# Optimization experiments

Hardware: AMD Instinct MI355X
Metric: run time of the kernel (lower is better)

The kernel has to match this reference:

```python
import jax, jax.numpy as jnp
import numpy as np

N = 100_000      # nodes
E = 1_600_000    # directed edges (before self-loops)
G = 128          # graphs in batch
IN = 32          # in_channels
HID = 32         # hidden_channels (per head)
HEADS = 4
SLOPE = 0.2      # GATConv leaky_relu negative_slope


def setup_inputs() -> dict:
    key = jax.random.key(0)
    ks = jax.random.split(key, 12)
    x = jax.random.normal(ks[0], (N, IN), jnp.float32)
    edge_index = jax.random.randint(ks[1], (2, E), 0, N)
    batch = jnp.sort(jax.random.randint(ks[2], (N,), 0, G))
    g = lambda k, sh: jax.random.normal(k, sh, jnp.float32) * (1.0 / np.sqrt(sh[0]))
    return {
        "x": x, "edge_index": edge_index, "batch": batch,
        # conv1: in -> heads*hid, concat
        "W1": g(ks[3], (IN, HEADS * HID)),
        "a_src1": jax.random.normal(ks[4], (HEADS, HID), jnp.float32) * 0.1,
        "a_dst1": jax.random.normal(ks[5], (HEADS, HID), jnp.float32) * 0.1,
        "b1": jnp.zeros((HEADS * HID,), jnp.float32),
        # conv2: heads*hid -> hid, heads=1, mean (concat=False)
        "W2": g(ks[6], (HEADS * HID, 1 * HID)),
        "a_src2": jax.random.normal(ks[7], (1, HID), jnp.float32) * 0.1,
        "a_dst2": jax.random.normal(ks[8], (1, HID), jnp.float32) * 0.1,
        "b2": jnp.zeros((HID,), jnp.float32),
        # classifier
        "Wc": g(ks[9], (HID, 1)),
        "bc": jnp.zeros((1,), jnp.float32),
    }


def _segment_softmax(e, seg, n):
    # e: [E', H]; softmax over edges sharing the same destination node
    m = jax.ops.segment_max(e, seg, num_segments=n)
    ex = jnp.exp(e - m[seg])
    den = jax.ops.segment_sum(ex, seg, num_segments=n)
    return ex / den[seg]


def _gat_layer(x, src, dst, W, a_src, a_dst, b, heads, ch, concat):
    n = x.shape[0]
    h = (x @ W).reshape(n, heads, ch)              # [N, H, C]
    e_src = jnp.sum(h * a_src, axis=-1)            # [N, H]
    e_dst = jnp.sum(h * a_dst, axis=-1)            # [N, H]
    e = jax.nn.leaky_relu(e_src[src] + e_dst[dst], SLOPE)   # [E', H]
    alpha = _segment_softmax(e, dst, n)            # [E', H]
    msg = h[src] * alpha[:, :, None]               # [E', H, C]
    out = jax.ops.segment_sum(msg, dst, num_segments=n)     # [N, H, C]
    out = out.reshape(n, heads * ch) if concat else out.mean(axis=1)
    return out + b


def reference(x, edge_index, batch, W1, a_src1, a_dst1, b1, W2, a_src2, a_dst2, b2, Wc, bc):
    n = x.shape[0]
    loops = jnp.arange(n, dtype=edge_index.dtype)  # GATConv add_self_loops=True
    src = jnp.concatenate([edge_index[0], loops])
    dst = jnp.concatenate([edge_index[1], loops])
    h = jax.nn.elu(_gat_layer(x, src, dst, W1, a_src1, a_dst1, b1, HEADS, HID, True))
    # dropout: eval mode -> identity
    h = jax.nn.elu(_gat_layer(h, src, dst, W2, a_src2, a_dst2, b2, 1, HID, False))
    # global_mean_pool over batch ids
    sums = jax.ops.segment_sum(h, batch, num_segments=G)
    cnt = jax.ops.segment_sum(jnp.ones((n, 1), h.dtype), batch, num_segments=G)
    pooled = sums / jnp.maximum(cnt, 1.0)
    return pooled @ Wc + bc                        # [G, 1]
```

## Files before the change

kernel.cpp:

```cpp
#include <hip/hip_runtime.h>
#include <math.h>

#define NT 100000
#define ET 1600000
#define GT 128
#define NBK 391
#define BSH 8
#define NBLK_A 256
#define CHUNK_A 6250

typedef float f4 __attribute__((ext_vector_type(4)));

__device__ __forceinline__ float lrelu(float v) { return v > 0.0f ? v : 0.2f * v; }
__device__ __forceinline__ float elu1(float v) { return v > 0.0f ? v : __expf(v) - 1.0f; }

__global__ __launch_bounds__(256) void k_histA(const int* __restrict__ dst, int* __restrict__ histA) {
  __shared__ int histL[NBK];
  int t = threadIdx.x, blk = blockIdx.x;
  for (int i = t; i < NBK; i += 256) histL[i] = 0;
  __syncthreads();
  int e0 = blk * CHUNK_A, e1 = min(ET, e0 + CHUNK_A);
  for (int e = e0 + t; e < e1; e += 256) atomicAdd(&histL[dst[e] >> BSH], 1);
  __syncthreads();
  for (int i = t; i < NBK; i += 256) histA[i * NBLK_A + blk] = histL[i];
}

__global__ __launch_bounds__(256) void k_scanB(int* __restrict__ histA, int* __restrict__ btot) {
  __shared__ int sh[256];
  int b = blockIdx.x, t = threadIdx.x;
  int v = histA[b * NBLK_A + t];
  sh[t] = v;
  __syncthreads();
  for (int off = 1; off < 256; off <<= 1) {
    int xv = (t >= off) ? sh[t - off] : 0;
    __syncthreads();
    sh[t] += xv;
    __syncthreads();
  }
  histA[b * NBLK_A + t] = sh[t] - v;
  if (t == 255) btot[b] = sh[255];
}

__global__ __launch_bounds__(512) void k_scanC(const int* __restrict__ btot, int* __restrict__ bbase) {
  __shared__ int sh[512];
  int t = threadIdx.x;
  int v = (t < NBK) ? btot[t] : 0;
  sh[t] = v;
  __syncthreads();
  for (int off = 1; off < 512; off <<= 1) {
    int xv = (t >= off) ? sh[t - off] : 0;
    __syncthreads();
    sh[t] += xv;
    __syncthreads();
  }
  if (t < NBK) bbase[t] = sh[t] - v;
  if (t == 0) bbase[NBK] = ET;
}

__global__ __launch_bounds__(256) void k_buck(const int* __restrict__ src, const int* __restrict__ dst,
                                              const int* __restrict__ histA, const int* __restrict__ bbase,
                                              int2* __restrict__ ebuf) {
  __shared__ int cur[NBK];
  int t = threadIdx.x, blk = blockIdx.x;
  for (int i = t; i < NBK; i += 256) cur[i] = histA[i * NBLK_A + blk] + bbase[i];
  __syncthreads();
  int e0 = blk * CHUNK_A, e1 = min(ET, e0 + CHUNK_A);
  for (int e = e0 + t; e < e1; e += 256) {
    int s = src[e], d = dst[e];
    int pos = atomicAdd(&cur[d >> BSH], 1);
    ebuf[pos] = make_int2(s, d);
  }
}

__global__ __launch_bounds__(256) void k_fine(const int2* __restrict__ ebuf, const int* __restrict__ bbase,
                                              int* __restrict__ rp, int* __restrict__ adj) {
  __shared__ int cnt[256];
  __shared__ int sh[256];
  __shared__ int cur[256];
  int b = blockIdx.x, t = threadIdx.x;
  int eb0 = bbase[b], eb1 = bbase[b + 1];
  cnt[t] = 0;
  __syncthreads();
  for (int e = eb0 + t; e < eb1; e += 256) atomicAdd(&cnt[ebuf[e].y & 255], 1);
  __syncthreads();
  int v = cnt[t];
  sh[t] = v;
  __syncthreads();
  for (int off = 1; off < 256; off <<= 1) {
    int xv = (t >= off) ? sh[t - off] : 0;
    __syncthreads();
    sh[t] += xv;
    __syncthreads();
  }
  int start = eb0 + sh[t] - v;
  cur[t] = start;
  int node = (b << BSH) + t;
  if (node < NT) rp[node] = start;
  if (node == NT - 1) rp[NT] = ET;
  __syncthreads();
  for (int e = eb0 + t; e < eb1; e += 256) {
    int2 p = ebuf[e];
    int pos = atomicAdd(&cur[p.y & 255], 1);
    adj[pos] = p.x;
  }
}

__global__ void k_prep(const float* __restrict__ W1, const float* __restrict__ as1,
                       const float* __restrict__ ad1, float* __restrict__ AB) {
  int t = threadIdx.x;
  int k = t >> 3, j = t & 7;
  const float* a = (j < 4) ? as1 : ad1;
  int h = j & 3;
  float s = 0.0f;
  for (int c = 0; c < 32; ++c) s += W1[k * 128 + h * 32 + c] * a[h * 32 + c];
  AB[t] = s;
}

__global__ __launch_bounds__(256) void k_att1(const float* __restrict__ x, const float* __restrict__ AB,
                                              float* __restrict__ es, float* __restrict__ ed) {
  __shared__ float xsh[32 * 33];
  __shared__ float absh[256];
  int t = threadIdx.x;
  int n0 = blockIdx.x * 32;
  absh[t] = AB[t];
  for (int i = t; i < 1024; i += 256) {
    int ln = i >> 5, k = i & 31;
    int node = n0 + ln;
    xsh[ln * 33 + k] = (node < NT) ? x[node * 32 + k] : 0.0f;
  }
  __syncthreads();
  int ln = t >> 3, j = t & 7;
  int node = n0 + ln;
  if (node < NT) {
    float s = 0.0f;
#pragma unroll
    for (int k = 0; k < 32; ++k) s += xsh[ln * 33 + k] * absh[k * 8 + j];
    if (j < 4) es[node * 4 + j] = s;
    else ed[node * 4 + (j - 4)] = s;
  }
}

__global__ __launch_bounds__(256) void k_agg1f(
    const int* __restrict__ rp, const int* __restrict__ adj,
    const float* __restrict__ es, const float* __restrict__ ed,
    const float* __restrict__ x,
    const float* __restrict__ W1, const float* __restrict__ b1,
    const float* __restrict__ W2,
    const float* __restrict__ as2, const float* __restrict__ ad2,
    float* __restrict__ h2, float* __restrict__ es2, float* __restrict__ ed2) {
  __shared__ int sbuf[8][34];
  __shared__ f4 wbufv[8][34];
  __shared__ float ysh[8][132];
  __shared__ float osh[8][132];
  int t = threadIdx.x;
  int wv = t >> 6, l = t & 63;
  int g = l >> 5, j = l & 31;
  int ns = wv * 2 + g;
  int n = blockIdx.x * 8 + ns;
  bool valid = (n < NT);
  int nc = valid ? n : NT - 1;
  const f4* es4 = (const f4*)es;
  int rs = rp[nc], re = rp[nc + 1];
  int deg = re - rs;
  f4 edn = ((const f4*)ed)[nc];
  f4 esn = es4[nc];
  float sv[4];
#pragma unroll
  for (int h = 0; h < 4; ++h) sv[h] = __expf(lrelu(esn[h] + edn[h]));
  int eg2 = j >> 3, q = j & 7;
  f4 a0 = {0,0,0,0}, a1 = {0,0,0,0}, a2 = {0,0,0,0}, a3 = {0,0,0,0};

  if (deg <= 32) {
    float ex[4] = {0.0f, 0.0f, 0.0f, 0.0f};
    if (j < deg) {
      int s = adj[rs + j];
      sbuf[ns][j] = s;
      f4 ev = es4[s];
#pragma unroll
      for (int h = 0; h < 4; ++h) ex[h] = __expf(lrelu(ev[h] + edn[h]));
    }
    float d[4] = {ex[0], ex[1], ex[2], ex[3]};
#pragma unroll
    for (int off = 1; off <= 16; off <<= 1)
#pragma unroll
      for (int h = 0; h < 4; ++h) d[h] += __shfl_xor(d[h], off);
    float inv[4];
#pragma unroll
    for (int h = 0; h < 4; ++h) inv[h] = 1.0f / (d[h] + sv[h]);
    if (j < deg) {
      f4 w4;
#pragma unroll
      for (int h = 0; h < 4; ++h) w4[h] = ex[h] * inv[h];
      wbufv[ns][j] = w4;
    }
    if (j == 0) {
      sbuf[ns][deg] = nc;
      f4 w4;
#pragma unroll
      for (int h = 0; h < 4; ++h) w4[h] = sv[h] * inv[h];
      wbufv[ns][deg] = w4;
    }
    __builtin_amdgcn_wave_barrier();
    for (int e = eg2; e <= deg; e += 4) {
      f4 xv = *(const f4*)&x[sbuf[ns][e] * 32 + 4 * q];
      f4 w4 = wbufv[ns][e];
      a0 += w4.x * xv; a1 += w4.y * xv; a2 += w4.z * xv; a3 += w4.w * xv;
    }
  } else {
    float d[4] = {0.0f, 0.0f, 0.0f, 0.0f};
    for (int jj = rs + j; jj < re; jj += 32) {
      f4 ev = es4[adj[jj]];
#pragma unroll
      for (int h = 0; h < 4; ++h) d[h] += __expf(lrelu(ev[h] + edn[h]));
    }
#pragma unroll
    for (int off = 1; off <= 16; off <<= 1)
#pragma unroll
      for (int h = 0; h < 4; ++h) d[h] += __shfl_xor(d[h], off);
    float inv[4];
#pragma unroll
    for (int h = 0; h < 4; ++h) inv[h] = 1.0f / (d[h] + sv[h]);
    for (int base = rs; base < re; base += 32) {
      int cnt = min(32, re - base);
      if (j < cnt) {
        int s = adj[base + j];
        sbuf[ns][j] = s;
        f4 ev = es4[s];
        f4 w4;
#pragma unroll
        for (int h = 0; h < 4; ++h) w4[h] = __expf(lrelu(ev[h] + edn[h])) * inv[h];
        wbufv[ns][j] = w4;
      }
      __builtin_amdgcn_wave_barrier();
      for (int e = eg2; e < cnt; e += 4) {
        f4 xv = *(const f4*)&x[sbuf[ns][e] * 32 + 4 * q];
        f4 w4 = wbufv[ns][e];
        a0 += w4.x * xv; a1 += w4.y * xv; a2 += w4.z * xv; a3 += w4.w * xv;
      }
      __builtin_amdgcn_wave_barrier();
    }
    if (eg2 == 0) {
      f4 xv = *(const f4*)&x[nc * 32 + 4 * q];
      a0 += sv[0] * inv[0] * xv; a1 += sv[1] * inv[1] * xv;
      a2 += sv[2] * inv[2] * xv; a3 += sv[3] * inv[3] * xv;
    }
  }

#pragma unroll
  for (int off = 8; off <= 16; off <<= 1) {
#pragma unroll
    for (int cc = 0; cc < 4; ++cc) {
      a0[cc] += __shfl_xor(a0[cc], off);
      a1[cc] += __shfl_xor(a1[cc], off);
      a2[cc] += __shfl_xor(a2[cc], off);
      a3[cc] += __shfl_xor(a3[cc], off);
    }
  }
  if (eg2 == 0) {
    *(f4*)&ysh[ns][0 * 33 + 4 * q] = a0;
    *(f4*)&ysh[ns][1 * 33 + 4 * q] = a1;
    *(f4*)&ysh[ns][2 * 33 + 4 * q] = a2;
    *(f4*)&ysh[ns][3 * 33 + 4 * q] = a3;
  }
  __syncthreads();

  {
    int ns2 = t >> 5, j2 = t & 31;
    int ch = j2 * 4, hh = j2 >> 3;
    f4 o = {0,0,0,0};
#pragma unroll
    for (int k = 0; k < 32; ++k) {
      o += ysh[ns2][hh * 33 + k] * *(const f4*)&W1[k * 128 + ch];
    }
    o += *(const f4*)&b1[ch];
#pragma unroll
    for (int cc = 0; cc < 4; ++cc) o[cc] = elu1(o[cc]);
    *(f4*)&osh[ns2][(ch >> 5) * 33 + (ch & 31)] = o;
  }
  __syncthreads();

  {
    int ns2 = t >> 5, j2 = t & 31;
    int kg = j2 >> 3, c4 = (j2 & 7) * 4;
    int n2 = blockIdx.x * 8 + ns2;
    bool v2 = (n2 < NT);
    f4 p = {0,0,0,0};
#pragma unroll
    for (int kk = 0; kk < 32; ++kk) {
      p += osh[ns2][kg * 33 + kk] * *(const f4*)&W2[(kg * 32 + kk) * 32 + c4];
    }
#pragma unroll
    for (int off = 8; off <= 16; off <<= 1)
#pragma unroll
      for (int cc = 0; cc < 4; ++cc) p[cc] += __shfl_xor(p[cc], off);
    if (kg == 0) {
      if (v2) *(f4*)&h2[n2 * 32 + c4] = p;
      f4 av = *(const f4*)&as2[c4];
      f4 dv = *(const f4*)&ad2[c4];
      float ps = p.x * av.x + p.y * av.y + p.z * av.z + p.w * av.w;
      float pd = p.x * dv.x + p.y * dv.y + p.z * dv.z + p.w * dv.w;
#pragma unroll
      for (int off = 1; off <= 4; off <<= 1) {
        ps += __shfl_xor(ps, off);
        pd += __shfl_xor(pd, off);
      }
      if ((j2 & 7) == 0 && v2) { es2[n2] = ps; ed2[n2] = pd; }
    }
  }
}

__global__ __launch_bounds__(256) void k_agg2(const int* __restrict__ rp, const int* __restrict__ adj,
                                              const float* __restrict__ es, const float* __restrict__ ed,
                                              const float* __restrict__ h, const float* __restrict__ b2,
                                              const float* __restrict__ Wc, float* __restrict__ z) {
  __shared__ int sbuf[8][34];
  __shared__ float wsh[8][34];
  int t = threadIdx.x;
  int wv = t >> 6, l = t & 63;
  int g = l >> 5, j = l & 31;
  int ns = wv * 2 + g;
  int n = blockIdx.x * 8 + ns;
  if (n >= NT) return;
  int rs = rp[n], re = rp[n + 1];
  int deg = re - rs;
  float edn = ed[n];
  float sv = __expf(lrelu(es[n] + edn));
  int eg2 = j >> 3, q = j & 7;
  f4 acc = {0,0,0,0};

  if (deg <= 32) {
    float ex = 0.0f;
    if (j < deg) {
      int s = adj[rs + j];
      sbuf[ns][j] = s;
      ex = __expf(lrelu(es[s] + edn));
    }
    float d = ex;
#pragma unroll
    for (int off = 1; off <= 16; off <<= 1) d += __shfl_xor(d, off);
    float inv = 1.0f / (d + sv);
    if (j < deg) wsh[ns][j] = ex * inv;
    if (j == 0) { sbuf[ns][deg] = n; wsh[ns][deg] = sv * inv; }
    __builtin_amdgcn_wave_barrier();
    for (int e = eg2; e <= deg; e += 4) {
      acc += wsh[ns][e] * *(const f4*)&h[sbuf[ns][e] * 32 + 4 * q];
    }
  } else {
    float d = 0.0f;
    for (int jj = rs + j; jj < re; jj += 32) d += __expf(lrelu(es[adj[jj]] + edn));
#pragma unroll
    for (int off = 1; off <= 16; off <<= 1) d += __shfl_xor(d, off);
    float inv = 1.0f / (d + sv);
    for (int base = rs; base < re; base += 32) {
      int cnt = min(32, re - base);
      if (j < cnt) {
        int s = adj[base + j];
        sbuf[ns][j] = s;
        wsh[ns][j] = __expf(lrelu(es[s] + edn)) * inv;
      }
      __builtin_amdgcn_wave_barrier();
      for (int e = eg2; e < cnt; e += 4) {
        acc += wsh[ns][e] * *(const f4*)&h[sbuf[ns][e] * 32 + 4 * q];
      }
      __builtin_amdgcn_wave_barrier();
    }
    if (eg2 == 0) acc += sv * inv * *(const f4*)&h[n * 32 + 4 * q];
  }

#pragma unroll
  for (int off = 8; off <= 16; off <<= 1)
#pragma unroll
    for (int cc = 0; cc < 4; ++cc) acc[cc] += __shfl_xor(acc[cc], off);
  if (eg2 == 0) {
    f4 o = acc + *(const f4*)&b2[4 * q];
#pragma unroll
    for (int cc = 0; cc < 4; ++cc) o[cc] = elu1(o[cc]);
    f4 wc = *(const f4*)&Wc[4 * q];
    float zz = o.x * wc.x + o.y * wc.y + o.z * wc.z + o.w * wc.w;
#pragma unroll
    for (int off = 1; off <= 4; off <<= 1) zz += __shfl_xor(zz, off);
    if (q == 0) z[n] = zz;
  }
}

__global__ __launch_bounds__(256) void k_poolz(const float* __restrict__ z, const int* __restrict__ batch,
                                               const float* __restrict__ bc, float* __restrict__ out) {
  int g = blockIdx.x;
  int lo = 0, hi = NT;
  while (lo < hi) { int mid = (lo + hi) >> 1; if (batch[mid] < g) lo = mid + 1; else hi = mid; }
  int start = lo;
  hi = NT;
  while (lo < hi) { int mid = (lo + hi) >> 1; if (batch[mid] < g + 1) lo = mid + 1; else hi = mid; }
  int end = lo;

  int t = threadIdx.x;
  float s = 0.0f;
  for (int n = start + t; n < end; n += 256) s += z[n];
#pragma unroll
  for (int off = 1; off <= 32; off <<= 1) s += __shfl_xor(s, off);
  __shared__ float sh[4];
  if ((t & 63) == 0) sh[t >> 6] = s;
  __syncthreads();
  if (t == 0) {
    float tot = sh[0] + sh[1] + sh[2] + sh[3];
    float cnt = (float)(end - start);
    out[g] = tot / fmaxf(cnt, 1.0f) + bc[0];
  }
}

extern "C" void kernel_launch(void* const* d_in, const int* in_sizes, int n_in,
                              void* d_out, int out_size, void* d_ws, size_t ws_size,
                              hipStream_t stream) {
  const float* x = (const float*)d_in[0];
  const int* ei = (const int*)d_in[1];
  const int* src = ei;
  const int* dst = ei + ET;
  const int* batch = (const int*)d_in[2];
  const float* W1 = (const float*)d_in[3];
  const float* asrc1 = (const float*)d_in[4];
  const float* adst1 = (const float*)d_in[5];
  const float* b1 = (const float*)d_in[6];
  const float* W2 = (const float*)d_in[7];
  const float* asrc2 = (const float*)d_in[8];
  const float* adst2 = (const float*)d_in[9];
  const float* b2 = (const float*)d_in[10];
  const float* Wc = (const float*)d_in[11];
  const float* bc = (const float*)d_in[12];
  float* out = (float*)d_out;
  char* ws = (char*)d_ws;

  int* row_ptr = (int*)(ws + 0);
  int* histA = (int*)(ws + 400128);
  int* btot = (int*)(ws + 800512);
  int* bbase = (int*)(ws + 802112);
  float* AB = (float*)(ws + 803712);
  int2* ebuf = (int2*)(ws + 804736);
  int* adj = (int*)(ws + 13604736);
  float* es1 = (float*)(ws + 20004736);
  float* ed1 = (float*)(ws + 21604736);
  float* es2 = (float*)(ws + 23204736);
  float* ed2 = (float*)(ws + 23604736);
  float* h2 = (float*)(ws + 24004736);
  float* z = (float*)(ws + 36804736);

  k_histA<<<NBLK_A, 256, 0, stream>>>(dst, histA);
  k_scanB<<<NBK, 256, 0, stream>>>(histA, btot);
  k_scanC<<<1, 512, 0, stream>>>(btot, bbase);
  k_buck<<<NBLK_A, 256, 0, stream>>>(src, dst, histA, bbase, ebuf);
  k_fine<<<NBK, 256, 0, stream>>>(ebuf, bbase, row_ptr, adj);

  k_prep<<<1, 256, 0, stream>>>(W1, asrc1, adst1, AB);
  k_att1<<<(NT + 31) / 32, 256, 0, stream>>>(x, AB, es1, ed1);

  k_agg1f<<<(NT + 7) / 8, 256, 0, stream>>>(row_ptr, adj, es1, ed1, x, W1, b1, W2,
                                            asrc2, adst2, h2, es2, ed2);

  k_agg2<<<(NT + 7) / 8, 256, 0, stream>>>(row_ptr, adj, es2, ed2, h2, b2, Wc, z);

  k_poolz<<<GT, 256, 0, stream>>>(z, batch, bc, out);
}
```

Measured before the change: 222.1 us.

## Pack bucketed edges into 32-bit words and restructure agg1 dense GEMVs

Edges are bucketed into single 32-bit words (17-bit source plus 8-bit local destination) instead of int2 pairs, halving the bytes written and read between the bucket and fine-sort passes. The per-block dense transforms in the layer-1 aggregation kernel are reorganised so each thread owns an output channel across all 8 nodes. Each W1/W2 weight is then loaded once per block and reused from registers, with a shuffle reduction over the k-split. A new shared buffer and extra barrier handle the layer-2 output and attention dot products, and the packing assumes node ids fit in 17 bits.

```diff
diff --git a/kernel.cpp b/kernel.cpp
--- a/kernel.cpp
+++ b/kernel.cpp
@@ -59,20 +59,21 @@
 
 __global__ __launch_bounds__(256) void k_buck(const int* __restrict__ src, const int* __restrict__ dst,
                                               const int* __restrict__ histA, const int* __restrict__ bbase,
-                                              int2* __restrict__ ebuf) {
+                                              unsigned int* __restrict__ ebuf) {
   __shared__ int cur[NBK];
   int t = threadIdx.x, blk = blockIdx.x;
   for (int i = t; i < NBK; i += 256) cur[i] = histA[i * NBLK_A + blk] + bbase[i];
   __syncthreads();
   int e0 = blk * CHUNK_A, e1 = min(ET, e0 + CHUNK_A);
   for (int e = e0 + t; e < e1; e += 256) {
-    int s = src[e], d = dst[e];
+    unsigned int s = (unsigned int)src[e];
+    int d = dst[e];
     int pos = atomicAdd(&cur[d >> BSH], 1);
-    ebuf[pos] = make_int2(s, d);
-  }
-}
-
-__global__ __launch_bounds__(256) void k_fine(const int2* __restrict__ ebuf, const int* __restrict__ bbase,
+    ebuf[pos] = ((unsigned int)(d & 255) << 17) | s;
+  }
+}
+
+__global__ __launch_bounds__(256) void k_fine(const unsigned int* __restrict__ ebuf, const int* __restrict__ bbase,
                                               int* __restrict__ rp, int* __restrict__ adj) {
   __shared__ int cnt[256];
   __shared__ int sh[256];
@@ -81,7 +82,7 @@
   int eb0 = bbase[b], eb1 = bbase[b + 1];
   cnt[t] = 0;
   __syncthreads();
-  for (int e = eb0 + t; e < eb1; e += 256) atomicAdd(&cnt[ebuf[e].y & 255], 1);
+  for (int e = eb0 + t; e < eb1; e += 256) atomicAdd(&cnt[ebuf[e] >> 17], 1);
   __syncthreads();
   int v = cnt[t];
   sh[t] = v;
@@ -99,9 +100,9 @@
   if (node == NT - 1) rp[NT] = ET;
   __syncthreads();
   for (int e = eb0 + t; e < eb1; e += 256) {
-    int2 p = ebuf[e];
-    int pos = atomicAdd(&cur[p.y & 255], 1);
-    adj[pos] = p.x;
+    unsigned int p = ebuf[e];
+    int pos = atomicAdd(&cur[p >> 17], 1);
+    adj[pos] = (int)(p & 0x1FFFFu);
   }
 }
 
@@ -151,7 +152,8 @@
   __shared__ int sbuf[8][34];
   __shared__ f4 wbufv[8][34];
   __shared__ float ysh[8][132];
-  __shared__ float osh[8][132];
+  __shared__ float osh[8][136];
+  __shared__ float psh[8][33];
   int t = threadIdx.x;
   int wv = t >> 6, l = t & 63;
   int g = l >> 5, j = l & 31;
@@ -265,46 +267,67 @@
   __syncthreads();
 
   {
-    int ns2 = t >> 5, j2 = t & 31;
-    int ch = j2 * 4, hh = j2 >> 3;
-    f4 o = {0,0,0,0};
-#pragma unroll
-    for (int k = 0; k < 32; ++k) {
-      o += ysh[ns2][hh * 33 + k] * *(const f4*)&W1[k * 128 + ch];
-    }
-    o += *(const f4*)&b1[ch];
-#pragma unroll
-    for (int cc = 0; cc < 4; ++cc) o[cc] = elu1(o[cc]);
-    *(f4*)&osh[ns2][(ch >> 5) * 33 + (ch & 31)] = o;
+    int kh = t & 1, c1 = t >> 1;
+    int h1 = c1 >> 5;
+    float o[8];
+#pragma unroll
+    for (int nd = 0; nd < 8; ++nd) o[nd] = 0.0f;
+#pragma unroll
+    for (int kk = 0; kk < 16; ++kk) {
+      int k = kh * 16 + kk;
+      float w = W1[k * 128 + c1];
+      int yi = h1 * 33 + k;
+#pragma unroll
+      for (int nd = 0; nd < 8; ++nd) o[nd] += ysh[nd][yi] * w;
+    }
+#pragma unroll
+    for (int nd = 0; nd < 8; ++nd) o[nd] += __shfl_xor(o[nd], 1);
+    if (kh == 0) {
+      float bb = b1[c1];
+      int cp = c1 + (c1 >> 4);
+#pragma unroll
+      for (int nd = 0; nd < 8; ++nd) osh[nd][cp] = elu1(o[nd] + bb);
+    }
   }
   __syncthreads();
 
   {
-    int ns2 = t >> 5, j2 = t & 31;
-    int kg = j2 >> 3, c4 = (j2 & 7) * 4;
-    int n2 = blockIdx.x * 8 + ns2;
-    bool v2 = (n2 < NT);
-    f4 p = {0,0,0,0};
-#pragma unroll
-    for (int kk = 0; kk < 32; ++kk) {
-      p += osh[ns2][kg * 33 + kk] * *(const f4*)&W2[(kg * 32 + kk) * 32 + c4];
-    }
-#pragma unroll
-    for (int off = 8; off <= 16; off <<= 1)
-#pragma unroll
-      for (int cc = 0; cc < 4; ++cc) p[cc] += __shfl_xor(p[cc], off);
+    int kg = t & 7, c2 = t >> 3;
+    float p[8];
+#pragma unroll
+    for (int nd = 0; nd < 8; ++nd) p[nd] = 0.0f;
+#pragma unroll
+    for (int kk = 0; kk < 16; ++kk) {
+      int k = kg * 16 + kk;
+      float w = W2[k * 32 + c2];
+      int kp = kg * 17 + kk;
+#pragma unroll
+      for (int nd = 0; nd < 8; ++nd) p[nd] += osh[nd][kp] * w;
+    }
+#pragma unroll
+    for (int off = 1; off <= 4; off <<= 1)
+#pragma unroll
+      for (int nd = 0; nd < 8; ++nd) p[nd] += __shfl_xor(p[nd], off);
     if (kg == 0) {
-      if (v2) *(f4*)&h2[n2 * 32 + c4] = p;
-      f4 av = *(const f4*)&as2[c4];
-      f4 dv = *(const f4*)&ad2[c4];
-      float ps = p.x * av.x + p.y * av.y + p.z * av.z + p.w * av.w;
-      float pd = p.x * dv.x + p.y * dv.y + p.z * dv.z + p.w * dv.w;
-#pragma unroll
-      for (int off = 1; off <= 4; off <<= 1) {
+#pragma unroll
+      for (int nd = 0; nd < 8; ++nd) psh[nd][c2] = p[nd];
+    }
+  }
+  __syncthreads();
+
+  {
+    int nd = t >> 5, j2 = t & 31;
+    int n2 = blockIdx.x * 8 + nd;
+    if (n2 < NT) {
+      float p = psh[nd][j2];
+      h2[n2 * 32 + j2] = p;
+      float ps = p * as2[j2], pd = p * ad2[j2];
+#pragma unroll
+      for (int off = 1; off <= 16; off <<= 1) {
         ps += __shfl_xor(ps, off);
         pd += __shfl_xor(pd, off);
       }
-      if ((j2 & 7) == 0 && v2) { es2[n2] = ps; ed2[n2] = pd; }
+      if (j2 == 0) { es2[n2] = ps; ed2[n2] = pd; }
     }
   }
 }
@@ -434,14 +457,14 @@
   int* btot = (int*)(ws + 800512);
   int* bbase = (int*)(ws + 802112);
   float* AB = (float*)(ws + 803712);
-  int2* ebuf = (int2*)(ws + 804736);
-  int* adj = (int*)(ws + 13604736);
-  float* es1 = (float*)(ws + 20004736);
-  float* ed1 = (float*)(ws + 21604736);
-  float* es2 = (float*)(ws + 23204736);
-  float* ed2 = (float*)(ws + 23604736);
-  float* h2 = (float*)(ws + 24004736);
-  float* z = (float*)(ws + 36804736);
+  unsigned int* ebuf = (unsigned int*)(ws + 804736);
+  int* adj = (int*)(ws + 7204736);
+  float* es1 = (float*)(ws + 13604736);
+  float* ed1 = (float*)(ws + 15204736);
+  float* es2 = (float*)(ws + 16804736);
+  float* ed2 = (float*)(ws + 17204736);
+  float* h2 = (float*)(ws + 17604736);
+  float* z = (float*)(ws + 30404736);
 
   k_histA<<<NBLK_A, 256, 0, stream>>>(dst, histA);
   k_scanB<<<NBK, 256, 0, stream>>>(histA, btot);
```

Measured after the change: 228.0 us. +2.7%, slower.
